# Kernel tuning notes

Hardware: AMD Instinct MI355X
Metric: run time of the kernel (lower is better)

## Reference

```python
import jax, jax.numpy as jnp
import numpy as np

N = 50000      # nodes
D = 128        # in_dim
O = 128        # out_dim
MAX_DEG = 32   # degrees uniform in [0, MAX_DEG]


def setup_inputs() -> dict:
    rng = np.random.default_rng(0)
    deg = rng.integers(0, MAX_DEG + 1, size=N)          # includes deg==0 nodes
    dst = np.repeat(np.arange(N), deg)                  # target node per edge (grouped, like the buckets)
    E = dst.shape[0]                                    # ~800000
    src = rng.integers(0, N, size=E)                    # neighbor index per edge (flat neighbor_list)

    key = jax.random.key(0)
    k1, k2, k3, k4 = jax.random.split(key, 4)
    scale = jnp.float32(1.0 / np.sqrt(D))
    return {
        "x":  jax.random.normal(k1, (N, D), jnp.float32),
        "Wg": jax.random.normal(k2, (O, D), jnp.float32) * scale,  # global_lin.weight
        "Wl": jax.random.normal(k3, (O, D), jnp.float32) * scale,  # local_lin.weight
        "Ws": jax.random.normal(k4, (O, D), jnp.float32) * scale,  # self_lin.weight
        "b":  jnp.zeros((O,), jnp.float32),                        # bias param
        "src": jnp.asarray(src, jnp.int32),
        "dst": jnp.asarray(dst, jnp.int32),
        "deg": jnp.asarray(deg, jnp.int32),
    }


def reference(x, Wg, Wl, Ws, b, src, dst, deg):
    n = x.shape[0]
    # global branch: applied to every node
    g_out = x @ Wg.T                                           # [N, O]
    # mean-aggregate neighbor features (gather + segment-sum == the per-bucket view().mean())
    neigh_sum = jax.ops.segment_sum(x[src], dst, num_segments=n)   # [N, D]
    degf = jnp.maximum(deg, 1).astype(x.dtype)[:, None]
    neigh_mean = neigh_sum * (1.0 / degf)                       # [N, D]
    # local + self branches only for deg > 0 (deg==0 bucket keeps just global_out)
    mask = (deg > 0).astype(x.dtype)[:, None]                   # [N, 1]
    out = g_out + mask * (neigh_mean @ Wl.T + x @ Ws.T) + b
    # dropout is identity in eval mode; ELU activation
    return jax.nn.elu(out)
```

## Files before the change

kernel.cpp:

```cpp
#include <hip/hip_runtime.h>
#include <cstdint>
#include <cstddef>

#define KCAT  384
#define AST   392
#define NPB   64

typedef __attribute__((ext_vector_type(8))) short bf16x8;
typedef __attribute__((ext_vector_type(4))) float f32x4;

static __device__ __forceinline__ unsigned short f2bf(float f) {
    unsigned int u = __builtin_bit_cast(unsigned int, f);
    unsigned int lsb = (u >> 16) & 1u;
    u += 0x7fffu + lsb;
    return (unsigned short)(u >> 16);
}
static __device__ __forceinline__ float bfhi(unsigned int u) {
    return __builtin_bit_cast(float, u & 0xFFFF0000u);
}
static __device__ __forceinline__ float bflo(unsigned int u) {
    return __builtin_bit_cast(float, u << 16);
}
static __device__ __forceinline__ void acc8(float* a, const uint4& v) {
    a[0] += bflo(v.x); a[1] += bfhi(v.x); a[2] += bflo(v.y); a[3] += bfhi(v.y);
    a[4] += bflo(v.z); a[5] += bfhi(v.z); a[6] += bflo(v.w); a[7] += bfhi(v.w);
}

__global__ void build_V(const float* __restrict__ Wg, const float* __restrict__ Wl,
                        const float* __restrict__ Ws, unsigned short* __restrict__ V) {
    const int o = blockIdx.x;
    const int k = threadIdx.x;
    float v;
    if (k < 128)      v = Wg[o * 128 + k];
    else if (k < 256) v = Wl[o * 128 + (k - 128)];
    else              v = Ws[o * 128 + (k - 256)];
    V[o * KCAT + k] = f2bf(v);
}

__global__ __launch_bounds__(256)
void convert_x(const float* __restrict__ x, unsigned short* __restrict__ xb, int total8) {
    int gid = blockIdx.x * 256 + threadIdx.x;
    if (gid >= total8) return;
    const float4* px = (const float4*)x + (size_t)gid * 2;
    float4 a = px[0], bq = px[1];
    uint4 u;
    u.x = (unsigned)f2bf(a.x)  | ((unsigned)f2bf(a.y)  << 16);
    u.y = (unsigned)f2bf(a.z)  | ((unsigned)f2bf(a.w)  << 16);
    u.z = (unsigned)f2bf(bq.x) | ((unsigned)f2bf(bq.y) << 16);
    u.w = (unsigned)f2bf(bq.z) | ((unsigned)f2bf(bq.w) << 16);
    ((uint4*)xb)[gid] = u;
}

__global__ __launch_bounds__(512, 6)
void fused_agg_gemm(const unsigned short* __restrict__ xb, const int* __restrict__ src,
                    const int* __restrict__ dst, const int* __restrict__ deg,
                    const unsigned short* __restrict__ V, const float* __restrict__ bias,
                    float* __restrict__ out, int N, int E) {
    __shared__ __align__(16) unsigned short Ash[NPB * AST];
    __shared__ int sstart[NPB];
    __shared__ int sdeg[NPB];
    const int t    = threadIdx.x;
    const int wv   = t >> 6;
    const int lane = t & 63;
    const int c    = lane & 15;
    const int p    = lane >> 4;
    const int base = blockIdx.x * NPB;

    if (wv == 0) {
        int lo = 0, hi = E;
        while (lo < hi) { int mid = (lo + hi) >> 1; if (dst[mid] < base) lo = mid + 1; else hi = mid; }
        int n  = base + lane;
        int dg = (n < N) ? deg[n] : 0;
        int incl = dg;
#pragma unroll
        for (int off = 1; off < 64; off <<= 1) {
            int v = __shfl_up(incl, off, 64);
            if (lane >= off) incl += v;
        }
        sstart[lane] = lo + incl - dg;
        sdeg[lane]   = dg;
    }
    __syncthreads();

    const uint4* x4 = (const uint4*)xb;
    for (int r = 0; r < 8; ++r) {
        const int row = wv * 8 + r;
        const int n   = base + row;
        const int d   = sdeg[row];
        const int s   = sstart[row];
        int idx = 0;
        if (lane < d) idx = src[s + lane];
        uint4 xv = {0, 0, 0, 0};
        if (p == 1 && n < N) xv = x4[(size_t)n * 16 + c];

        float a[8] = {0,0,0,0,0,0,0,0};
        float b[8] = {0,0,0,0,0,0,0,0};
        for (int g = 0; g * 16 < d; ++g) {
            int e0 = g * 16 + p;
            int r0 = __shfl(idx, e0, 64);
            int r1 = __shfl(idx, e0 + 4, 64);
            int r2 = __shfl(idx, e0 + 8, 64);
            int r3 = __shfl(idx, e0 + 12, 64);
            uint4 v0 = x4[(size_t)r0 * 16 + c];
            uint4 v1 = x4[(size_t)r1 * 16 + c];
            uint4 v2 = x4[(size_t)r2 * 16 + c];
            uint4 v3 = x4[(size_t)r3 * 16 + c];
            if (e0 < d)      acc8(a, v0);
            if (e0 + 4 < d)  acc8(b, v1);
            if (e0 + 8 < d)  acc8(a, v2);
            if (e0 + 12 < d) acc8(b, v3);
        }
#pragma unroll
        for (int i = 0; i < 8; ++i) a[i] += b[i];
#pragma unroll
        for (int i = 0; i < 8; ++i) {
            a[i] += __shfl_xor(a[i], 16, 64);
            a[i] += __shfl_xor(a[i], 32, 64);
        }
        unsigned short* arow = Ash + row * AST;
        if (p == 0) {
            float inv = (d > 0) ? 1.0f / (float)d : 0.0f;
            uint4 u;
            u.x = (unsigned)f2bf(a[0]*inv) | ((unsigned)f2bf(a[1]*inv) << 16);
            u.y = (unsigned)f2bf(a[2]*inv) | ((unsigned)f2bf(a[3]*inv) << 16);
            u.z = (unsigned)f2bf(a[4]*inv) | ((unsigned)f2bf(a[5]*inv) << 16);
            u.w = (unsigned)f2bf(a[6]*inv) | ((unsigned)f2bf(a[7]*inv) << 16);
            *(uint4*)(arow + 128 + c * 8) = u;
        } else if (p == 1) {
            *(uint4*)(arow + c * 8) = xv;
            uint4 z = xv;
            if (d == 0) { z.x = 0; z.y = 0; z.z = 0; z.w = 0; }
            *(uint4*)(arow + 256 + c * 8) = z;
        }
    }
    __syncthreads();

    const int wrow = (wv >> 2) * 32;
    const int wcol = (wv & 3) * 32;
    const int quad = lane >> 4;
    const unsigned short* V0 = V + (size_t)(wcol + c) * KCAT + quad * 8;
    const unsigned short* V1 = V + (size_t)(wcol + 16 + c) * KCAT + quad * 8;

    f32x4 acc[2][2];
#pragma unroll
    for (int i = 0; i < 2; ++i)
#pragma unroll
        for (int j = 0; j < 2; ++j) acc[i][j] = (f32x4){0.f, 0.f, 0.f, 0.f};

    bf16x8 b0 = *(const bf16x8*)V0;
    bf16x8 b1 = *(const bf16x8*)V1;
    for (int k0 = 0; k0 < KCAT; k0 += 32) {
        int kn = (k0 + 32 < KCAT) ? k0 + 32 : 0;
        bf16x8 n0 = *(const bf16x8*)(V0 + kn);
        bf16x8 n1 = *(const bf16x8*)(V1 + kn);
        bf16x8 a0 = *(const bf16x8*)(Ash + (size_t)(wrow + c) * AST + k0 + quad * 8);
        bf16x8 a1 = *(const bf16x8*)(Ash + (size_t)(wrow + 16 + c) * AST + k0 + quad * 8);
        acc[0][0] = __builtin_amdgcn_mfma_f32_16x16x32_bf16(a0, b0, acc[0][0], 0, 0, 0);
        acc[0][1] = __builtin_amdgcn_mfma_f32_16x16x32_bf16(a0, b1, acc[0][1], 0, 0, 0);
        acc[1][0] = __builtin_amdgcn_mfma_f32_16x16x32_bf16(a1, b0, acc[1][0], 0, 0, 0);
        acc[1][1] = __builtin_amdgcn_mfma_f32_16x16x32_bf16(a1, b1, acc[1][1], 0, 0, 0);
        b0 = n0; b1 = n1;
    }

#pragma unroll
    for (int ri = 0; ri < 2; ++ri) {
#pragma unroll
        for (int ci = 0; ci < 2; ++ci) {
            int col = wcol + ci * 16 + c;
            float bv = bias[col];
#pragma unroll
            for (int reg = 0; reg < 4; ++reg) {
                int grow = base + wrow + ri * 16 + quad * 4 + reg;
                if (grow < N) {
                    float v = acc[ri][ci][reg] + bv;
                    out[(size_t)grow * 128 + col] = (v > 0.f) ? v : expm1f(v);
                }
            }
        }
    }
}

extern "C" void kernel_launch(void* const* d_in, const int* in_sizes, int n_in,
                              void* d_out, int out_size, void* d_ws, size_t ws_size,
                              hipStream_t stream) {
    const float* x  = (const float*)d_in[0];
    const float* Wg = (const float*)d_in[1];
    const float* Wl = (const float*)d_in[2];
    const float* Ws = (const float*)d_in[3];
    const float* b  = (const float*)d_in[4];
    const int*   src = (const int*)d_in[5];
    const int*   dst = (const int*)d_in[6];
    const int*   deg = (const int*)d_in[7];
    const int E = in_sizes[5];
    const int N = in_sizes[7];
    float* out = (float*)d_out;

    unsigned short* V  = (unsigned short*)d_ws;
    unsigned short* xb = (unsigned short*)((char*)d_ws + 98304);

    build_V<<<dim3(128), dim3(KCAT), 0, stream>>>(Wg, Wl, Ws, V);
    int total8 = N * 16;
    convert_x<<<dim3((total8 + 255) / 256), dim3(256), 0, stream>>>(x, xb, total8);
    fused_agg_gemm<<<dim3((N + NPB - 1) / NPB), dim3(512), 0, stream>>>(
        xb, src, dst, deg, V, b, out, N, E);
}
```

Baseline: 160.5 us.

## Shrink node tiles, precompute block edge offsets, and merge prep kernels

Cuts the nodes per block from 64 to 16 and uses 256-thread blocks, giving many more, smaller blocks to raise occupancy and balance the irregular gather. The per-block binary search over dst moves into a merged prep kernel that also builds the weight matrix and converts x to bf16, removing a launch. The neighbor gather is unrolled into at most two 16-edge chunks, with index loads hoisted ahead of the loop. In exchange, the full weight matrix is reread from global/L2 by four times as many blocks, and degrees above 32 are no longer handled.

```diff
diff --git a/kernel.cpp b/kernel.cpp
--- a/kernel.cpp
+++ b/kernel.cpp
@@ -4,7 +4,8 @@
 
 #define KCAT  384
 #define AST   392
-#define NPB   64
+#define NPB   16
+#define PREPV 128
 
 typedef __attribute__((ext_vector_type(8))) short bf16x8;
 typedef __attribute__((ext_vector_type(4))) float f32x4;
@@ -26,36 +27,47 @@
     a[4] += bflo(v.z); a[5] += bfhi(v.z); a[6] += bflo(v.w); a[7] += bfhi(v.w);
 }
 
-__global__ void build_V(const float* __restrict__ Wg, const float* __restrict__ Wl,
-                        const float* __restrict__ Ws, unsigned short* __restrict__ V) {
-    const int o = blockIdx.x;
-    const int k = threadIdx.x;
-    float v;
-    if (k < 128)      v = Wg[o * 128 + k];
-    else if (k < 256) v = Wl[o * 128 + (k - 128)];
-    else              v = Ws[o * 128 + (k - 256)];
-    V[o * KCAT + k] = f2bf(v);
-}
-
 __global__ __launch_bounds__(256)
-void convert_x(const float* __restrict__ x, unsigned short* __restrict__ xb, int total8) {
-    int gid = blockIdx.x * 256 + threadIdx.x;
-    if (gid >= total8) return;
-    const float4* px = (const float4*)x + (size_t)gid * 2;
-    float4 a = px[0], bq = px[1];
-    uint4 u;
-    u.x = (unsigned)f2bf(a.x)  | ((unsigned)f2bf(a.y)  << 16);
-    u.y = (unsigned)f2bf(a.z)  | ((unsigned)f2bf(a.w)  << 16);
-    u.z = (unsigned)f2bf(bq.x) | ((unsigned)f2bf(bq.y) << 16);
-    u.w = (unsigned)f2bf(bq.z) | ((unsigned)f2bf(bq.w) << 16);
-    ((uint4*)xb)[gid] = u;
-}
-
-__global__ __launch_bounds__(512, 6)
+void prep(const float* __restrict__ x, const float* __restrict__ Wg,
+          const float* __restrict__ Wl, const float* __restrict__ Ws,
+          const int* __restrict__ dst, unsigned short* __restrict__ V,
+          unsigned short* __restrict__ xb, int* __restrict__ blkoff,
+          int total8, int nblk, int noffb, int E) {
+    const int bx = blockIdx.x;
+    const int t  = threadIdx.x;
+    if (bx < PREPV) {
+        const int o = bx;
+        float v = (t < 128) ? Wg[o * 128 + t] : Wl[o * 128 + (t - 128)];
+        V[o * KCAT + t] = f2bf(v);
+        if (t < 128) V[o * KCAT + 256 + t] = f2bf(Ws[o * 128 + t]);
+    } else if (bx < PREPV + noffb) {
+        int b = (bx - PREPV) * 256 + t;
+        if (b < nblk) {
+            int target = b * NPB;
+            int lo = 0, hi = E;
+            while (lo < hi) { int mid = (lo + hi) >> 1; if (dst[mid] < target) lo = mid + 1; else hi = mid; }
+            blkoff[b] = lo;
+        }
+    } else {
+        int gid = (bx - PREPV - noffb) * 256 + t;
+        if (gid < total8) {
+            const float4* px = (const float4*)x + (size_t)gid * 2;
+            float4 a = px[0], bq = px[1];
+            uint4 u;
+            u.x = (unsigned)f2bf(a.x)  | ((unsigned)f2bf(a.y)  << 16);
+            u.y = (unsigned)f2bf(a.z)  | ((unsigned)f2bf(a.w)  << 16);
+            u.z = (unsigned)f2bf(bq.x) | ((unsigned)f2bf(bq.y) << 16);
+            u.w = (unsigned)f2bf(bq.z) | ((unsigned)f2bf(bq.w) << 16);
+            ((uint4*)xb)[gid] = u;
+        }
+    }
+}
+
+__global__ __launch_bounds__(256, 8)
 void fused_agg_gemm(const unsigned short* __restrict__ xb, const int* __restrict__ src,
-                    const int* __restrict__ dst, const int* __restrict__ deg,
+                    const int* __restrict__ deg, const int* __restrict__ blkoff,
                     const unsigned short* __restrict__ V, const float* __restrict__ bias,
-                    float* __restrict__ out, int N, int E) {
+                    float* __restrict__ out, int N) {
     __shared__ __align__(16) unsigned short Ash[NPB * AST];
     __shared__ int sstart[NPB];
     __shared__ int sdeg[NPB];
@@ -67,40 +79,59 @@
     const int base = blockIdx.x * NPB;
 
     if (wv == 0) {
-        int lo = 0, hi = E;
-        while (lo < hi) { int mid = (lo + hi) >> 1; if (dst[mid] < base) lo = mid + 1; else hi = mid; }
+        int lo = blkoff[blockIdx.x];
         int n  = base + lane;
-        int dg = (n < N) ? deg[n] : 0;
+        int dg = (lane < NPB && n < N) ? deg[n] : 0;
         int incl = dg;
 #pragma unroll
-        for (int off = 1; off < 64; off <<= 1) {
+        for (int off = 1; off < NPB; off <<= 1) {
             int v = __shfl_up(incl, off, 64);
             if (lane >= off) incl += v;
         }
-        sstart[lane] = lo + incl - dg;
-        sdeg[lane]   = dg;
+        if (lane < NPB) { sstart[lane] = lo + incl - dg; sdeg[lane] = dg; }
     }
     __syncthreads();
 
     const uint4* x4 = (const uint4*)xb;
-    for (int r = 0; r < 8; ++r) {
-        const int row = wv * 8 + r;
+    int dgs[4], sss[4], idxs[4];
+#pragma unroll
+    for (int r = 0; r < 4; ++r) {
+        int row = wv * 4 + r;
+        dgs[r] = sdeg[row];
+        sss[r] = sstart[row];
+        idxs[r] = 0;
+        if (lane < dgs[r]) idxs[r] = src[sss[r] + lane];
+    }
+#pragma unroll
+    for (int r = 0; r < 4; ++r) {
+        const int row = wv * 4 + r;
         const int n   = base + row;
-        const int d   = sdeg[row];
-        const int s   = sstart[row];
-        int idx = 0;
-        if (lane < d) idx = src[s + lane];
+        const int d   = dgs[r];
         uint4 xv = {0, 0, 0, 0};
         if (p == 1 && n < N) xv = x4[(size_t)n * 16 + c];
 
         float a[8] = {0,0,0,0,0,0,0,0};
         float b[8] = {0,0,0,0,0,0,0,0};
-        for (int g = 0; g * 16 < d; ++g) {
-            int e0 = g * 16 + p;
-            int r0 = __shfl(idx, e0, 64);
-            int r1 = __shfl(idx, e0 + 4, 64);
-            int r2 = __shfl(idx, e0 + 8, 64);
-            int r3 = __shfl(idx, e0 + 12, 64);
+        {
+            int r0 = __shfl(idxs[r], p, 64);
+            int r1 = __shfl(idxs[r], p + 4, 64);
+            int r2 = __shfl(idxs[r], p + 8, 64);
+            int r3 = __shfl(idxs[r], p + 12, 64);
+            uint4 v0 = x4[(size_t)r0 * 16 + c];
+            uint4 v1 = x4[(size_t)r1 * 16 + c];
+            uint4 v2 = x4[(size_t)r2 * 16 + c];
+            uint4 v3 = x4[(size_t)r3 * 16 + c];
+            if (p < d)      acc8(a, v0);
+            if (p + 4 < d)  acc8(b, v1);
+            if (p + 8 < d)  acc8(a, v2);
+            if (p + 12 < d) acc8(b, v3);
+        }
+        if (d > 16) {
+            int e0 = 16 + p;
+            int r0 = __shfl(idxs[r], e0, 64);
+            int r1 = __shfl(idxs[r], e0 + 4, 64);
+            int r2 = __shfl(idxs[r], e0 + 8, 64);
+            int r3 = __shfl(idxs[r], e0 + 12, 64);
             uint4 v0 = x4[(size_t)r0 * 16 + c];
             uint4 v1 = x4[(size_t)r1 * 16 + c];
             uint4 v2 = x4[(size_t)r2 * 16 + c];
@@ -135,47 +166,35 @@
     }
     __syncthreads();
 
-    const int wrow = (wv >> 2) * 32;
-    const int wcol = (wv & 3) * 32;
     const int quad = lane >> 4;
+    const int wcol = wv * 32;
     const unsigned short* V0 = V + (size_t)(wcol + c) * KCAT + quad * 8;
     const unsigned short* V1 = V + (size_t)(wcol + 16 + c) * KCAT + quad * 8;
 
-    f32x4 acc[2][2];
-#pragma unroll
-    for (int i = 0; i < 2; ++i)
-#pragma unroll
-        for (int j = 0; j < 2; ++j) acc[i][j] = (f32x4){0.f, 0.f, 0.f, 0.f};
-
+    f32x4 acc0 = (f32x4){0.f, 0.f, 0.f, 0.f};
+    f32x4 acc1 = (f32x4){0.f, 0.f, 0.f, 0.f};
     bf16x8 b0 = *(const bf16x8*)V0;
     bf16x8 b1 = *(const bf16x8*)V1;
     for (int k0 = 0; k0 < KCAT; k0 += 32) {
         int kn = (k0 + 32 < KCAT) ? k0 + 32 : 0;
         bf16x8 n0 = *(const bf16x8*)(V0 + kn);
         bf16x8 n1 = *(const bf16x8*)(V1 + kn);
-        bf16x8 a0 = *(const bf16x8*)(Ash + (size_t)(wrow + c) * AST + k0 + quad * 8);
-        bf16x8 a1 = *(const bf16x8*)(Ash + (size_t)(wrow + 16 + c) * AST + k0 + quad * 8);
-        acc[0][0] = __builtin_amdgcn_mfma_f32_16x16x32_bf16(a0, b0, acc[0][0], 0, 0, 0);
-        acc[0][1] = __builtin_amdgcn_mfma_f32_16x16x32_bf16(a0, b1, acc[0][1], 0, 0, 0);
-        acc[1][0] = __builtin_amdgcn_mfma_f32_16x16x32_bf16(a1, b0, acc[1][0], 0, 0, 0);
-        acc[1][1] = __builtin_amdgcn_mfma_f32_16x16x32_bf16(a1, b1, acc[1][1], 0, 0, 0);
+        bf16x8 a0 = *(const bf16x8*)(Ash + (size_t)c * AST + k0 + quad * 8);
+        acc0 = __builtin_amdgcn_mfma_f32_16x16x32_bf16(a0, b0, acc0, 0, 0, 0);
+        acc1 = __builtin_amdgcn_mfma_f32_16x16x32_bf16(a0, b1, acc1, 0, 0, 0);
         b0 = n0; b1 = n1;
     }
 
-#pragma unroll
-    for (int ri = 0; ri < 2; ++ri) {
-#pragma unroll
-        for (int ci = 0; ci < 2; ++ci) {
-            int col = wcol + ci * 16 + c;
-            float bv = bias[col];
-#pragma unroll
-            for (int reg = 0; reg < 4; ++reg) {
-                int grow = base + wrow + ri * 16 + quad * 4 + reg;
-                if (grow < N) {
-                    float v = acc[ri][ci][reg] + bv;
-                    out[(size_t)grow * 128 + col] = (v > 0.f) ? v : expm1f(v);
-                }
-            }
+    const int col0 = wcol + c, col1 = wcol + 16 + c;
+    const float bv0 = bias[col0], bv1 = bias[col1];
+#pragma unroll
+    for (int reg = 0; reg < 4; ++reg) {
+        int grow = base + quad * 4 + reg;
+        if (grow < N) {
+            float v0 = acc0[reg] + bv0;
+            float v1 = acc1[reg] + bv1;
+            out[(size_t)grow * 128 + col0] = (v0 > 0.f) ? v0 : expm1f(v0);
+            out[(size_t)grow * 128 + col1] = (v1 > 0.f) ? v1 : expm1f(v1);
         }
     }
 }
@@ -195,12 +214,17 @@
     const int N = in_sizes[7];
     float* out = (float*)d_out;
 
-    unsigned short* V  = (unsigned short*)d_ws;
-    unsigned short* xb = (unsigned short*)((char*)d_ws + 98304);
-
-    build_V<<<dim3(128), dim3(KCAT), 0, stream>>>(Wg, Wl, Ws, V);
-    int total8 = N * 16;
-    convert_x<<<dim3((total8 + 255) / 256), dim3(256), 0, stream>>>(x, xb, total8);
-    fused_agg_gemm<<<dim3((N + NPB - 1) / NPB), dim3(512), 0, stream>>>(
-        xb, src, dst, deg, V, b, out, N, E);
-}
+    unsigned short* V      = (unsigned short*)d_ws;
+    int*            blkoff = (int*)((char*)d_ws + 98304);
+    unsigned short* xb     = (unsigned short*)((char*)d_ws + 98304 + 16384);
+
+    const int nblk   = (N + NPB - 1) / NPB;
+    const int noffb  = (nblk + 255) / 256;
+    const int total8 = N * 16;
+    const int nconv  = (total8 + 255) / 256;
+
+    prep<<<dim3(PREPV + noffb + nconv), dim3(256), 0, stream>>>(
+        x, Wg, Wl, Ws, dst, V, xb, blkoff, total8, nblk, noffb, E);
+    fused_agg_gemm<<<dim3(nblk), dim3(256), 0, stream>>>(
+        xb, src, deg, blkoff, V, b, out, N);
+}
```

After: 168.7 us. 1.05x slower.
